# Kernel tuning notes

Hardware: AMD Instinct MI355X
Metric: run time of the kernel (lower is better)

The kernel has to match this reference:

```python
import jax, jax.numpy as jnp
import numpy as np

DIM = 128
B = 8
HM, WM = 64, 64  # target (m) spatial size


def setup_inputs() -> dict:
    key = jax.random.key(0)
    ks = jax.random.split(key, 20)
    d = DIM
    sc = 1.0 / np.sqrt(d)       # GRU / 1x1-conv fan-in scale
    sc_in = 1.0 / np.sqrt(3 * d)
    f32 = jnp.float32
    return {
        'l': jax.random.normal(ks[0], (B, d, 2 * HM, 2 * WM), f32),
        'm': jax.random.normal(ks[1], (B, d, HM, WM), f32),
        's': jax.random.normal(ks[2], (B, d, HM // 2, WM // 2), f32),
        'proj_in_w': jax.random.normal(ks[3], (d, 3 * d), f32) * sc_in,
        'proj_in_scale': jax.random.uniform(ks[4], (d,), f32, 0.5, 1.5),
        'proj_in_shift': jax.random.normal(ks[5], (d,), f32) * 0.1,
        'wih_h': jax.random.normal(ks[6], (3 * d, d), f32) * sc,
        'whh_h': jax.random.normal(ks[7], (3 * d, d), f32) * sc,
        'bih_h': jax.random.normal(ks[8], (3 * d,), f32) * 0.05,
        'bhh_h': jax.random.normal(ks[9], (3 * d,), f32) * 0.05,
        'wih_w': jax.random.normal(ks[10], (3 * d, d), f32) * sc,
        'whh_w': jax.random.normal(ks[11], (3 * d, d), f32) * sc,
        'bih_w': jax.random.normal(ks[12], (3 * d,), f32) * 0.05,
        'bhh_w': jax.random.normal(ks[13], (3 * d,), f32) * 0.05,
        'gate_w': jax.random.normal(ks[14], (d, d), f32) * sc,
        'gate_b': jax.random.normal(ks[15], (d,), f32) * 0.05,
        'proj_out_w': jax.random.normal(ks[16], (d, d), f32) * sc,
        'proj_out_scale': jax.random.uniform(ks[17], (d,), f32, 0.5, 1.5),
        'proj_out_shift': jax.random.normal(ks[18], (d,), f32) * 0.1,
    }


def _conv_bn_relu(x, w, scale, shift):
    # 1x1 conv (no bias) + folded BatchNorm (per-channel affine) + ReLU
    y = jnp.einsum('bchw,oc->bohw', x, w)
    return jax.nn.relu(y * scale[None, :, None, None] + shift[None, :, None, None])


def _gru_scan(x_seq, wih, whh, bih, bhh):
    # x_seq: [T, N, d]; PyTorch GRUCell gate layout: r | z | n
    T, N, _ = x_seq.shape
    d = whh.shape[1]
    gx = jnp.einsum('tnc,gc->tng', x_seq, wih) + bih  # input gates precomputed

    def step(h, gx_t):
        gh = h @ whh.T + bhh
        r = jax.nn.sigmoid(gx_t[:, :d] + gh[:, :d])
        z = jax.nn.sigmoid(gx_t[:, d:2 * d] + gh[:, d:2 * d])
        n = jnp.tanh(gx_t[:, 2 * d:] + r * gh[:, 2 * d:])
        h_new = (1.0 - z) * n + z * h
        return h_new, h_new

    h0 = jnp.zeros((N, d), x_seq.dtype)
    _, out = jax.lax.scan(step, h0, gx)
    return out  # [T, N, d]


def _forward(l, m, s, proj_in_w, proj_in_scale, proj_in_shift,
             wih_h, whh_h, bih_h, bhh_h, wih_w, whh_w, bih_w, bhh_w,
             gate_w, gate_b, proj_out_w, proj_out_scale, proj_out_shift):
    b, _, H, W = m.shape
    lr = jax.image.resize(l, (b, l.shape[1], H, W), 'bilinear')  # align_corners=False
    sr = jax.image.resize(s, (b, s.shape[1], H, W), 'bilinear')
    x = _conv_bn_relu(jnp.concatenate([lr, m, sr], axis=1),
                      proj_in_w, proj_in_scale, proj_in_shift)  # [b,c,H,W]
    c = x.shape[1]

    # vertical scan: sequence over H, batch (b, W)
    xh = jnp.transpose(x, (2, 0, 3, 1)).reshape(H, b * W, c)
    oh = _gru_scan(xh, wih_h, whh_h, bih_h, bhh_h).reshape(H, b, W, c)
    oh = jnp.transpose(oh, (1, 3, 0, 2))  # [b,c,H,W]

    # horizontal scan: sequence over W, batch (b, H)
    xw = jnp.transpose(x, (3, 0, 2, 1)).reshape(W, b * H, c)
    ow = _gru_scan(xw, wih_w, whh_w, bih_w, bhh_w).reshape(W, b, H, c)
    ow = jnp.transpose(ow, (1, 3, 2, 0))  # [b,c,H,W]

    scanned = oh + ow
    gate = jax.nn.sigmoid(jnp.einsum('bchw,oc->bohw', scanned, gate_w)
                          + gate_b[None, :, None, None])
    gated = scanned * gate
    return _conv_bn_relu(gated, proj_out_w, proj_out_scale, proj_out_shift) + x


def reference(l, m, s, proj_in_w, proj_in_scale, proj_in_shift,
              wih_h, whh_h, bih_h, bhh_h, wih_w, whh_w, bih_w, bhh_w,
              gate_w, gate_b, proj_out_w, proj_out_scale, proj_out_shift):
    return _forward(l, m, s, proj_in_w, proj_in_scale, proj_in_shift,
                    wih_h, whh_h, bih_h, bhh_h, wih_w, whh_w, bih_w, bhh_w,
                    gate_w, gate_b, proj_out_w, proj_out_scale, proj_out_shift)
```

## Files before the change

### kernel.cpp

```cpp
#include <hip/hip_runtime.h>


typedef __bf16 bf16;
typedef _Float16 f16;
typedef __attribute__((ext_vector_type(8))) __bf16 bf16x8;
typedef __attribute__((ext_vector_type(4))) __bf16 bf16x4;
typedef __attribute__((ext_vector_type(4))) _Float16 f16x4;
typedef __attribute__((ext_vector_type(4))) float f32x4;
typedef __attribute__((ext_vector_type(2))) float f32x2;

__device__ __forceinline__ f32x4 mfma16(bf16x8 a, bf16x8 b, f32x4 c) {
  return __builtin_amdgcn_mfma_f32_16x16x32_bf16(a, b, c, 0, 0, 0);
}
__device__ __forceinline__ float sigm(float x) { return 1.0f / (1.0f + __expf(-x)); }
__device__ __forceinline__ float tanh_fast(float x) {
  float e = __expf(2.0f * x);
  return 1.0f - 2.0f / (e + 1.0f);
}

__global__ __launch_bounds__(256) void k_prep(
    const float* __restrict__ wpi, const float* __restrict__ wihh,
    const float* __restrict__ whhh, const float* __restrict__ wihw,
    const float* __restrict__ whhw, const float* __restrict__ wg,
    const float* __restrict__ wpo, bf16* __restrict__ dst) {
  int i = blockIdx.x * 256 + threadIdx.x;
  if (i < 49152) dst[i] = (bf16)wpi[i];
  else if (i < 98304) dst[i] = (bf16)wihh[i - 49152];
  else if (i < 147456) dst[i] = (bf16)whhh[i - 98304];
  else if (i < 196608) dst[i] = (bf16)wihw[i - 147456];
  else if (i < 245760) dst[i] = (bf16)whhw[i - 196608];
  else if (i < 262144) dst[i] = (bf16)wg[i - 245760];
  else if (i < 278528) dst[i] = (bf16)wpo[i - 262144];
}

__global__ __launch_bounds__(512, 2) void k_projin(
    const float* __restrict__ lp, const float* __restrict__ mp,
    const float* __restrict__ sp, const float* __restrict__ pscale,
    const float* __restrict__ pshift, const bf16* __restrict__ Wpi,
    f16* __restrict__ xf16, bf16* __restrict__ xb, bf16* __restrict__ xbT) {
  __shared__ __align__(16) bf16 xin[64][392];
  const int tid = threadIdx.x;
  const int bb = blockIdx.x >> 6;
  const int h = blockIdx.x & 63;

  {
    const int wq = tid & 63, cq = tid >> 6;
    float wy[4]; int iy[4];
    {
      float ssum = 0.f;
#pragma unroll
      for (int dy = 0; dy < 4; ++dy) {
        int y = 2 * h - 1 + dy;
        bool ok = (y >= 0) && (y < 128);
        iy[dy] = ok ? y : 0;
        float w0 = (dy == 0 || dy == 3) ? 0.125f : 0.375f;
        wy[dy] = ok ? w0 : 0.f;
        ssum += wy[dy];
      }
      float inv = 1.f / ssum;
#pragma unroll
      for (int dy = 0; dy < 4; ++dy) wy[dy] *= inv;
    }
    float wx[4];
    {
      float ssum = 0.f;
#pragma unroll
      for (int dx = 0; dx < 4; ++dx) {
        int xq = 2 * wq - 1 + dx;
        bool ok = (xq >= 0) && (xq < 128);
        float w0 = (dx == 0 || dx == 3) ? 0.125f : 0.375f;
        wx[dx] = ok ? w0 : 0.f;
        ssum += wx[dx];
      }
      float inv = 1.f / ssum;
#pragma unroll
      for (int dx = 0; dx < 4; ++dx) wx[dx] *= inv;
    }
    int syA, syB; float wsyA, wsyB;
    {
      int j0 = (h - 1) >> 1;
      float f = (h & 1) ? 0.25f : 0.75f;
      float a = 1.f - f, b2 = f;
      if (j0 < 0) a = 0.f;
      if (j0 + 1 > 31) b2 = 0.f;
      float inv = 1.f / (a + b2);
      wsyA = a * inv; wsyB = b2 * inv;
      syA = j0 < 0 ? 0 : j0;
      syB = (j0 + 1 > 31) ? 31 : (j0 + 1);
    }
    int sxA, sxB; float wsxA, wsxB;
    {
      int j0 = (wq - 1) >> 1;
      float f = (wq & 1) ? 0.25f : 0.75f;
      float a = 1.f - f, b2 = f;
      if (j0 < 0) a = 0.f;
      if (j0 + 1 > 31) b2 = 0.f;
      float inv = 1.f / (a + b2);
      wsxA = a * inv; wsxB = b2 * inv;
      sxA = j0 < 0 ? 0 : j0;
      sxB = (j0 + 1 > 31) ? 31 : (j0 + 1);
    }
#pragma unroll 4
    for (int ci = 0; ci < 16; ++ci) {
      int c = cq * 16 + ci;
      const float* lc = lp + ((size_t)(bb * 128 + c) << 14);
      float acc = 0.f;
#pragma unroll
      for (int dy = 0; dy < 4; ++dy) {
        const float* row = lc + (iy[dy] << 7);
        f32x2 v = *(const f32x2*)&row[2 * wq];
        float bprev = __shfl_up(v.y, 1);
        float anext = __shfl_down(v.x, 1);
        float rs = wx[0] * bprev + wx[1] * v.x + wx[2] * v.y + wx[3] * anext;
        acc = fmaf(wy[dy], rs, acc);
      }
      xin[wq][c] = (bf16)acc;
      xin[wq][128 + c] = (bf16)mp[((bb * 128 + c) * 64 + h) * 64 + wq];
      const float* sc = sp + ((size_t)(bb * 128 + c) << 10);
      float sv = wsyA * (wsxA * sc[(syA << 5) + sxA] + wsxB * sc[(syA << 5) + sxB]) +
                 wsyB * (wsxA * sc[(syB << 5) + sxA] + wsxB * sc[(syB << 5) + sxB]);
      xin[wq][256 + c] = (bf16)sv;
    }
  }
  __syncthreads();

  const int lane = tid & 63, wv = tid >> 6;
  const int l16 = lane & 15, k8 = (lane >> 4) * 8, j4 = (lane >> 4) * 4;
  const f32x4 zf = {0.f, 0.f, 0.f, 0.f};
  f32x4 acc[4];
#pragma unroll
  for (int pt = 0; pt < 4; ++pt) acc[pt] = zf;

  for (int kk = 0; kk < 12; ++kk) {
    bf16x8 bfr[4];
#pragma unroll
    for (int pt = 0; pt < 4; ++pt)
      bfr[pt] = *(const bf16x8*)&xin[pt * 16 + l16][kk * 32 + k8];
    bf16x8 afr = *(const bf16x8*)(Wpi + (size_t)(wv * 16 + l16) * 384 + kk * 32 + k8);
#pragma unroll
    for (int pt = 0; pt < 4; ++pt) acc[pt] = mfma16(afr, bfr[pt], acc[pt]);
  }
  {
    int c0 = wv * 16 + j4;
    f32x4 scv = *(const f32x4*)&pscale[c0];
    f32x4 shv = *(const f32x4*)&pshift[c0];
#pragma unroll
    for (int pt = 0; pt < 4; ++pt) {
      int pw = pt * 16 + l16;
      bf16x4 pk;
#pragma unroll
      for (int j = 0; j < 4; ++j) {
        float v = fmaxf(acc[pt][j] * scv[j] + shv[j], 0.f);
        xf16[(size_t)((bb * 128 + c0 + j) * 64 + h) * 64 + pw] = (f16)v;
        pk[j] = (bf16)v;
      }
      *(bf16x4*)&xb[(size_t)(bb * 4096 + h * 64 + pw) * 128 + c0] = pk;
      *(bf16x4*)&xbT[(size_t)(bb * 4096 + pw * 64 + h) * 128 + c0] = pk;
    }
  }
}

__global__ __launch_bounds__(512, 2) void k_gx(
    const bf16* __restrict__ xb, const bf16* __restrict__ xbT,
    const bf16* __restrict__ wih_h_b, const bf16* __restrict__ wih_w_b,
    const float* __restrict__ bih_h, const float* __restrict__ bih_w,
    const float* __restrict__ bhh_h, const float* __restrict__ bhh_w,
    f16* __restrict__ gxh, f16* __restrict__ gxw) {
  const int dir = blockIdx.z;
  const int nb = blockIdx.y;
  const int t0 = blockIdx.x * 2;
  const bf16* xsrc = dir ? xbT : xb;
  const bf16* wih = dir ? wih_w_b : wih_h_b;
  const float* bih = dir ? bih_w : bih_h;
  const float* bhh = dir ? bhh_w : bhh_h;
  f16* gx = dir ? gxw : gxh;

  const int tid = threadIdx.x, lane = tid & 63, w = tid >> 6;
  const int l16 = lane & 15, k8 = (lane >> 4) * 8, j4 = (lane >> 4) * 4;
  const int n = nb * 16 + l16;
  const int pb = n >> 6, q = n & 63;

  bf16x8 afr[3][4];
#pragma unroll
  for (int part = 0; part < 3; ++part) {
    int gbase = part * 128 + w * 16;
#pragma unroll
    for (int kk = 0; kk < 4; ++kk)
      afr[part][kk] = *(const bf16x8*)(wih + (size_t)(gbase + l16) * 128 + kk * 32 + k8);
  }
  const f32x4 zf = {0.f, 0.f, 0.f, 0.f};
  f32x4 acc[3][2];
#pragma unroll
  for (int part = 0; part < 3; ++part) { acc[part][0] = zf; acc[part][1] = zf; }

#pragma unroll
  for (int pt = 0; pt < 2; ++pt) {
    const bf16* xr = xsrc + (size_t)(pb * 4096 + (t0 + pt) * 64 + q) * 128;
#pragma unroll
    for (int kk = 0; kk < 4; ++kk) {
      bf16x8 bfr = *(const bf16x8*)(xr + kk * 32 + k8);
#pragma unroll
      for (int part = 0; part < 3; ++part)
        acc[part][pt] = mfma16(afr[part][kk], bfr, acc[part][pt]);
    }
  }
#pragma unroll
  for (int part = 0; part < 3; ++part) {
    int g0 = part * 128 + w * 16 + j4;
    f32x4 bi = *(const f32x4*)&bih[g0];
    if (part < 2) {
      f32x4 bh = *(const f32x4*)&bhh[g0];
#pragma unroll
      for (int j = 0; j < 4; ++j) bi[j] += bh[j];
    }
#pragma unroll
    for (int pt = 0; pt < 2; ++pt) {
      f16x4 pk;
#pragma unroll
      for (int j = 0; j < 4; ++j) pk[j] = (f16)(acc[part][pt][j] + bi[j]);
      *(f16x4*)&gx[((size_t)(((t0 + pt) * 32 + nb) * 3 + part) * 512 + tid) * 4] = pk;
    }
  }
}

__global__ __launch_bounds__(512, 2) void k_scan(
    const bf16* __restrict__ whh_h_b, const bf16* __restrict__ whh_w_b,
    const float* __restrict__ bhh_h, const float* __restrict__ bhh_w,
    const f16* __restrict__ gxh, const f16* __restrict__ gxw,
    f16* __restrict__ ohb, f16* __restrict__ owb) {
  const int dir = blockIdx.x >> 5;
  const int nb = blockIdx.x & 31;
  const bf16* whh = dir ? whh_w_b : whh_h_b;
  const float* bhh = dir ? bhh_w : bhh_h;
  const f16* gx = dir ? gxw : gxh;
  f16* outb = dir ? owb : ohb;

  __shared__ __align__(16) bf16 hbuf[2][16][136];

  const int tid = threadIdx.x, lane = tid & 63, w = tid >> 6;
  const int l16 = lane & 15, k8 = (lane >> 4) * 8, j4 = (lane >> 4) * 4;
  const int cc0 = w * 16 + j4;

  bf16x8 afr[3][4];
#pragma unroll
  for (int part = 0; part < 3; ++part) {
    int gbase = part * 128 + w * 16;
#pragma unroll
    for (int kk = 0; kk < 4; ++kk)
      afr[part][kk] = *(const bf16x8*)(whh + (size_t)(gbase + l16) * 128 + kk * 32 + k8);
  }
  const f32x4 bhn = *(const f32x4*)&bhh[256 + cc0];

  for (int i = tid; i < 2 * 16 * 136; i += 512) ((bf16*)hbuf)[i] = (bf16)0.f;

  const int n = nb * 16 + l16;
  const int pb = n >> 6, q = n & 63;
  const int pbase0 = pb * 4096 + (dir ? q * 64 : q);
  const int pstep = dir ? 1 : 64;

  f16x4 gxr, gxz, gxn;
  {
    const size_t b0 = ((size_t)nb * 3) * 512 + tid;
    gxr = *(const f16x4*)&gx[(b0) * 4];
    gxz = *(const f16x4*)&gx[(b0 + 512) * 4];
    gxn = *(const f16x4*)&gx[(b0 + 1024) * 4];
  }
  f32x4 hreg = {0.f, 0.f, 0.f, 0.f};
  int cur = 0;
  __syncthreads();

  const f32x4 zf = {0.f, 0.f, 0.f, 0.f};
  for (int t = 0; t < 64; ++t) {
    f16x4 gxr_n, gxz_n, gxn_n;
    {
      int tn = t < 63 ? t + 1 : 63;
      const size_t b0 = ((size_t)(tn * 32 + nb) * 3) * 512 + tid;
      gxr_n = *(const f16x4*)&gx[(b0) * 4];
      gxz_n = *(const f16x4*)&gx[(b0 + 512) * 4];
      gxn_n = *(const f16x4*)&gx[(b0 + 1024) * 4];
    }
    bf16x8 hb[4];
#pragma unroll
    for (int kk = 0; kk < 4; ++kk)
      hb[kk] = *(const bf16x8*)&hbuf[cur][l16][kk * 32 + k8];
    f32x4 aR = zf, aZ = zf, aN = zf;
#pragma unroll
    for (int kk = 0; kk < 4; ++kk) {
      aR = mfma16(afr[0][kk], hb[kk], aR);
      aZ = mfma16(afr[1][kk], hb[kk], aZ);
      aN = mfma16(afr[2][kk], hb[kk], aN);
    }
    bf16x4 hb4;
    f16x4 o4;
#pragma unroll
    for (int j = 0; j < 4; ++j) {
      float r = sigm((float)gxr[j] + aR[j]);
      float z = sigm((float)gxz[j] + aZ[j]);
      float nn = tanh_fast((float)gxn[j] + r * (aN[j] + bhn[j]));
      float h = nn + z * (hreg[j] - nn);
      hreg[j] = h;
      hb4[j] = (bf16)h;
      o4[j] = (f16)h;
    }
    *(bf16x4*)&hbuf[cur ^ 1][l16][cc0] = hb4;
    *(f16x4*)&outb[(size_t)(pbase0 + t * pstep) * 128 + cc0] = o4;
    asm volatile("s_waitcnt lgkmcnt(0)\n\ts_barrier" ::: "memory");
    cur ^= 1;
    gxr = gxr_n; gxz = gxz_n; gxn = gxn_n;
  }
}

__global__ __launch_bounds__(256, 2) void k_final(
    const f16* __restrict__ ohb, const f16* __restrict__ owb,
    const bf16* __restrict__ Wg, const float* __restrict__ gate_b,
    const bf16* __restrict__ Wpo, const float* __restrict__ poscale,
    const float* __restrict__ poshift, const f16* __restrict__ xf16,
    float* __restrict__ out) {
  __shared__ __align__(16) float sf[64][132];
  __shared__ __align__(16) bf16 sb[64][136];
  __shared__ __align__(16) bf16 gbuf[64][136];
  const int tid = threadIdx.x;
  const int bb = blockIdx.x >> 6, h = blockIdx.x & 63;
  const int pbase = bb * 4096 + h * 64;
  for (int i = tid; i < 8192; i += 256) {
    int w = i >> 7, cc = i & 127;
    size_t idx = (size_t)(pbase + w) * 128 + cc;
    float v = (float)ohb[idx] + (float)owb[idx];
    sf[w][cc] = v;
    sb[w][cc] = (bf16)v;
  }
  __syncthreads();
  const int lane = tid & 63, wv = tid >> 6;
  const int l16 = lane & 15, k8 = (lane >> 4) * 8, j4 = (lane >> 4) * 4;
  const f32x4 zf = {0.f, 0.f, 0.f, 0.f};
  f32x4 acc[2][4];
#pragma unroll
  for (int i = 0; i < 2; ++i)
#pragma unroll
    for (int pt = 0; pt < 4; ++pt) acc[i][pt] = zf;
#pragma unroll
  for (int kk = 0; kk < 4; ++kk) {
    bf16x8 bfr[4];
#pragma unroll
    for (int pt = 0; pt < 4; ++pt)
      bfr[pt] = *(const bf16x8*)&sb[pt * 16 + l16][kk * 32 + k8];
#pragma unroll
    for (int i = 0; i < 2; ++i) {
      bf16x8 afr = *(const bf16x8*)(Wg + (size_t)((wv * 2 + i) * 16 + l16) * 128 + kk * 32 + k8);
#pragma unroll
      for (int pt = 0; pt < 4; ++pt) acc[i][pt] = mfma16(afr, bfr[pt], acc[i][pt]);
    }
  }
#pragma unroll
  for (int i = 0; i < 2; ++i) {
    int o0 = (wv * 2 + i) * 16 + j4;
    f32x4 gb4 = *(const f32x4*)&gate_b[o0];
#pragma unroll
    for (int pt = 0; pt < 4; ++pt) {
      int pc = pt * 16 + l16;
      f32x4 sv = *(const f32x4*)&sf[pc][o0];
      bf16x4 pk;
#pragma unroll
      for (int j = 0; j < 4; ++j) {
        float g = sigm(acc[i][pt][j] + gb4[j]);
        pk[j] = (bf16)(sv[j] * g);
      }
      *(bf16x4*)&gbuf[pc][o0] = pk;
    }
  }
  __syncthreads();
  f32x4 acc2[2][4];
#pragma unroll
  for (int i = 0; i < 2; ++i)
#pragma unroll
    for (int pt = 0; pt < 4; ++pt) acc2[i][pt] = zf;
#pragma unroll
  for (int kk = 0; kk < 4; ++kk) {
    bf16x8 bfr[4];
#pragma unroll
    for (int pt = 0; pt < 4; ++pt)
      bfr[pt] = *(const bf16x8*)&gbuf[pt * 16 + l16][kk * 32 + k8];
#pragma unroll
    for (int i = 0; i < 2; ++i) {
      bf16x8 afr = *(const bf16x8*)(Wpo + (size_t)((wv * 2 + i) * 16 + l16) * 128 + kk * 32 + k8);
#pragma unroll
      for (int pt = 0; pt < 4; ++pt) acc2[i][pt] = mfma16(afr, bfr[pt], acc2[i][pt]);
    }
  }
#pragma unroll
  for (int i = 0; i < 2; ++i) {
    int o0 = (wv * 2 + i) * 16 + j4;
    f32x4 scv = *(const f32x4*)&poscale[o0];
    f32x4 shv = *(const f32x4*)&poshift[o0];
#pragma unroll
    for (int pt = 0; pt < 4; ++pt) {
      int pc = pt * 16 + l16;
#pragma unroll
      for (int j = 0; j < 4; ++j) {
        int oc = o0 + j;
        size_t oi = (size_t)((bb * 128 + oc) * 64 + h) * 64 + pc;
        float v = fmaxf(acc2[i][pt][j] * scv[j] + shv[j], 0.f) + (float)xf16[oi];
        out[oi] = v;
      }
    }
  }
}

extern "C" void kernel_launch(void* const* d_in, const int* in_sizes, int n_in,
                              void* d_out, int out_size, void* d_ws, size_t ws_size,
                              hipStream_t stream) {
  const float* lp = (const float*)d_in[0];
  const float* mp = (const float*)d_in[1];
  const float* sp = (const float*)d_in[2];
  const float* proj_in_w = (const float*)d_in[3];
  const float* proj_in_scale = (const float*)d_in[4];
  const float* proj_in_shift = (const float*)d_in[5];
  const float* wih_h = (const float*)d_in[6];
  const float* whh_h = (const float*)d_in[7];
  const float* bih_h = (const float*)d_in[8];
  const float* bhh_h = (const float*)d_in[9];
  const float* wih_w = (const float*)d_in[10];
  const float* whh_w = (const float*)d_in[11];
  const float* bih_w = (const float*)d_in[12];
  const float* bhh_w = (const float*)d_in[13];
  const float* gate_w = (const float*)d_in[14];
  const float* gate_b = (const float*)d_in[15];
  const float* proj_out_w = (const float*)d_in[16];
  const float* proj_out_scale = (const float*)d_in[17];
  const float* proj_out_shift = (const float*)d_in[18];
  float* out = (float*)d_out;

  char* ws = (char*)d_ws;
  bf16* wb = (bf16*)ws;
  bf16* Wpi_b = wb + 0;
  bf16* Wih_h_b = wb + 49152;
  bf16* Whh_h_b = wb + 98304;
  bf16* Wih_w_b = wb + 147456;
  bf16* Whh_w_b = wb + 196608;
  bf16* Wg_b = wb + 245760;
  bf16* Wpo_b = wb + 262144;
  f16* xf16 = (f16*)(ws + 557056);
  bf16* xb = (bf16*)(ws + 8945664);
  bf16* xbT = (bf16*)(ws + 17334272);
  f16* gxh = (f16*)(ws + 25722880);
  f16* gxw = (f16*)(ws + 50888704);
  f16* ohb = (f16*)(ws + 76054528);
  f16* owb = (f16*)(ws + 84443136);

  k_prep<<<dim3(1088), dim3(256), 0, stream>>>(proj_in_w, wih_h, whh_h, wih_w,
                                               whh_w, gate_w, proj_out_w, wb);
  k_projin<<<dim3(512), dim3(512), 0, stream>>>(lp, mp, sp, proj_in_scale,
                                                proj_in_shift, Wpi_b, xf16, xb, xbT);
  k_gx<<<dim3(32, 32, 2), dim3(512), 0, stream>>>(xb, xbT, Wih_h_b, Wih_w_b,
                                                  bih_h, bih_w, bhh_h, bhh_w,
                                                  gxh, gxw);
  k_scan<<<dim3(64), dim3(512), 0, stream>>>(Whh_h_b, Whh_w_b, bhh_h, bhh_w,
                                             gxh, gxw, ohb, owb);
  k_final<<<dim3(512), dim3(256), 0, stream>>>(ohb, owb, Wg_b, gate_b, Wpo_b,
                                               proj_out_scale, proj_out_shift,
                                               xf16, out);
}
```

Before: 293.0 us.

## Deepen gx prefetch in GRU scan, unroll by four, vectorize final-stage loads

The GRU scan loop is unrolled by four and now prefetches the precomputed input gates two timesteps ahead through a four-slot register ring, instead of one step ahead. This gives global loads more latency slack on the serial recurrence. The per-step barrier is wrapped in sched_barrier fences so the compiler cannot move work across it. Separately, the final kernel's load of the two scan outputs is widened to 4-element f16 vectors, with vectorized LDS stores. These changes add register pressure in exchange.

```diff
diff --git a/kernel.cpp b/kernel.cpp
--- a/kernel.cpp
+++ b/kernel.cpp
@@ -258,55 +258,64 @@
   const int pbase0 = pb * 4096 + (dir ? q * 64 : q);
   const int pstep = dir ? 1 : 64;
 
-  f16x4 gxr, gxz, gxn;
-  {
-    const size_t b0 = ((size_t)nb * 3) * 512 + tid;
-    gxr = *(const f16x4*)&gx[(b0) * 4];
-    gxz = *(const f16x4*)&gx[(b0 + 512) * 4];
-    gxn = *(const f16x4*)&gx[(b0 + 1024) * 4];
+  f16x4 gq[4][3];
+#pragma unroll
+  for (int tp = 0; tp < 2; ++tp) {
+    const size_t b0 = ((size_t)(tp * 32 + nb) * 3) * 512 + tid;
+    gq[tp][0] = *(const f16x4*)&gx[b0 * 4];
+    gq[tp][1] = *(const f16x4*)&gx[(b0 + 512) * 4];
+    gq[tp][2] = *(const f16x4*)&gx[(b0 + 1024) * 4];
   }
   f32x4 hreg = {0.f, 0.f, 0.f, 0.f};
-  int cur = 0;
-  __syncthreads();
+
+  __builtin_amdgcn_sched_barrier(0);
+  asm volatile("s_waitcnt lgkmcnt(0)");
+  __builtin_amdgcn_s_barrier();
+  __builtin_amdgcn_sched_barrier(0);
 
   const f32x4 zf = {0.f, 0.f, 0.f, 0.f};
-  for (int t = 0; t < 64; ++t) {
-    f16x4 gxr_n, gxz_n, gxn_n;
-    {
-      int tn = t < 63 ? t + 1 : 63;
-      const size_t b0 = ((size_t)(tn * 32 + nb) * 3) * 512 + tid;
-      gxr_n = *(const f16x4*)&gx[(b0) * 4];
-      gxz_n = *(const f16x4*)&gx[(b0 + 512) * 4];
-      gxn_n = *(const f16x4*)&gx[(b0 + 1024) * 4];
-    }
-    bf16x8 hb[4];
-#pragma unroll
-    for (int kk = 0; kk < 4; ++kk)
-      hb[kk] = *(const bf16x8*)&hbuf[cur][l16][kk * 32 + k8];
-    f32x4 aR = zf, aZ = zf, aN = zf;
-#pragma unroll
-    for (int kk = 0; kk < 4; ++kk) {
-      aR = mfma16(afr[0][kk], hb[kk], aR);
-      aZ = mfma16(afr[1][kk], hb[kk], aZ);
-      aN = mfma16(afr[2][kk], hb[kk], aN);
-    }
-    bf16x4 hb4;
-    f16x4 o4;
-#pragma unroll
-    for (int j = 0; j < 4; ++j) {
-      float r = sigm((float)gxr[j] + aR[j]);
-      float z = sigm((float)gxz[j] + aZ[j]);
-      float nn = tanh_fast((float)gxn[j] + r * (aN[j] + bhn[j]));
-      float h = nn + z * (hreg[j] - nn);
-      hreg[j] = h;
-      hb4[j] = (bf16)h;
-      o4[j] = (f16)h;
-    }
-    *(bf16x4*)&hbuf[cur ^ 1][l16][cc0] = hb4;
-    *(f16x4*)&outb[(size_t)(pbase0 + t * pstep) * 128 + cc0] = o4;
-    asm volatile("s_waitcnt lgkmcnt(0)\n\ts_barrier" ::: "memory");
-    cur ^= 1;
-    gxr = gxr_n; gxz = gxz_n; gxn = gxn_n;
+  for (int tb = 0; tb < 16; ++tb) {
+#pragma unroll
+    for (int u = 0; u < 4; ++u) {
+      const int t = tb * 4 + u;
+      {
+        int tp = t + 2 < 64 ? t + 2 : 63;
+        const size_t b0 = ((size_t)(tp * 32 + nb) * 3) * 512 + tid;
+        gq[(u + 2) & 3][0] = *(const f16x4*)&gx[b0 * 4];
+        gq[(u + 2) & 3][1] = *(const f16x4*)&gx[(b0 + 512) * 4];
+        gq[(u + 2) & 3][2] = *(const f16x4*)&gx[(b0 + 1024) * 4];
+      }
+      const int cur = u & 1;
+      bf16x8 hb[4];
+#pragma unroll
+      for (int kk = 0; kk < 4; ++kk)
+        hb[kk] = *(const bf16x8*)&hbuf[cur][l16][kk * 32 + k8];
+      f32x4 aR = zf, aZ = zf, aN = zf;
+#pragma unroll
+      for (int kk = 0; kk < 4; ++kk) {
+        aR = mfma16(afr[0][kk], hb[kk], aR);
+        aZ = mfma16(afr[1][kk], hb[kk], aZ);
+        aN = mfma16(afr[2][kk], hb[kk], aN);
+      }
+      bf16x4 hb4;
+      f16x4 o4;
+#pragma unroll
+      for (int j = 0; j < 4; ++j) {
+        float r = sigm((float)gq[u][0][j] + aR[j]);
+        float z = sigm((float)gq[u][1][j] + aZ[j]);
+        float nn = tanh_fast((float)gq[u][2][j] + r * (aN[j] + bhn[j]));
+        float h = nn + z * (hreg[j] - nn);
+        hreg[j] = h;
+        hb4[j] = (bf16)h;
+        o4[j] = (f16)h;
+      }
+      *(bf16x4*)&hbuf[cur ^ 1][l16][cc0] = hb4;
+      *(f16x4*)&outb[(size_t)(pbase0 + t * pstep) * 128 + cc0] = o4;
+      __builtin_amdgcn_sched_barrier(0);
+      asm volatile("s_waitcnt lgkmcnt(0)");
+      __builtin_amdgcn_s_barrier();
+      __builtin_amdgcn_sched_barrier(0);
+    }
   }
 }
 
@@ -322,12 +331,20 @@
   const int tid = threadIdx.x;
   const int bb = blockIdx.x >> 6, h = blockIdx.x & 63;
   const int pbase = bb * 4096 + h * 64;
-  for (int i = tid; i < 8192; i += 256) {
-    int w = i >> 7, cc = i & 127;
-    size_t idx = (size_t)(pbase + w) * 128 + cc;
-    float v = (float)ohb[idx] + (float)owb[idx];
-    sf[w][cc] = v;
-    sb[w][cc] = (bf16)v;
+  for (int i = tid; i < 2048; i += 256) {
+    int w = i >> 5, cg = (i & 31) * 4;
+    size_t idx = (size_t)(pbase + w) * 128 + cg;
+    f16x4 a = *(const f16x4*)&ohb[idx];
+    f16x4 b = *(const f16x4*)&owb[idx];
+    f32x4 v;
+    bf16x4 pk;
+#pragma unroll
+    for (int j = 0; j < 4; ++j) {
+      v[j] = (float)a[j] + (float)b[j];
+      pk[j] = (bf16)v[j];
+    }
+    *(f32x4*)&sf[w][cg] = v;
+    *(bf16x4*)&sb[w][cg] = pk;
   }
   __syncthreads();
   const int lane = tid & 63, wv = tid >> 6;
```

Result: no change. 287.9 us (-1.7%).
